# Performance work log

Measured on AMD Instinct MI355X. Metric: run time of the kernel, lower is better.

## Reference

```python
import jax, jax.numpy as jnp
import numpy as np

T0 = 16
EPS = 1.1920929e-07  # torch fp32 finfo eps used by F.rms_norm default

def rmsnorm(v):
    return v * jax.lax.rsqrt(jnp.mean(v * v, axis=-1, keepdims=True) + EPS)

def apply_rotary_emb(x, cos, sin):
    # x: (B, S, H, C); rotate-half style as in source
    d = x.shape[-1] // 2
    x1, x2 = x[..., :d], x[..., d:]
    return jnp.concatenate([x1 * cos + x2 * sin, -x1 * sin + x2 * cos], axis=-1)

def setup_inputs():
    key = jax.random.key(0)
    ks = jax.random.split(key, 8)
    B, T, C, H = 8, 8192, 128, 8
    S = (T0 // 4) * T0 + 1  # 64 selected tokens + 1 sink = 65
    x = jax.random.normal(ks[0], (B, T, C), jnp.float32)
    # RoPE tables over the sink-augmented attention sequence, head_dim/2 = 64
    inv = 1.0 / (10000.0 ** (jnp.arange(C // 2, dtype=jnp.float32) / (C // 2)))
    ang = jnp.arange(S, dtype=jnp.float32)[:, None] * inv[None, :]
    cos = jnp.cos(ang)[None, :, None, :]  # (1, 65, 1, 64)
    sin = jnp.sin(ang)[None, :, None, :]
    sink = 0.02 * jax.random.normal(ks[1], (1, H, C), jnp.float32)
    W_qkvg = 0.02 * jax.random.normal(ks[2], (4 * C * H, C), jnp.float32)
    patch_w = 0.02 * jax.random.normal(ks[3], (T0 * C,), jnp.float32)
    W_out = 0.02 * jax.random.normal(ks[4], (C, H * C), jnp.float32)
    tao = jnp.array([1.2, 1.2], jnp.float32)
    return {"x": x, "cos": cos, "sin": sin, "sink": sink, "W_qkvg": W_qkvg,
            "patch_w": patch_w, "W_out": W_out, "tao": tao}

def reference(x, cos, sin, sink, W_qkvg, patch_w, W_out, tao):
    B, T, C = x.shape
    H = sink.shape[1]
    Np = T // T0  # T chosen as multiple of T0, so pad P = 0
    # --- patch scoring + topk patch selection (patch_toks) ---
    xp = x.reshape(B, Np, T0 * C)
    score = jax.nn.softmax(rmsnorm(xp) @ patch_w, axis=-1)  # (B, Np)
    _, I = jax.lax.top_k(score, T0 // 4)                    # top 4 patches
    I = jnp.sort(I, axis=-1)                                # (B, 4)
    # --- qkvg projection over ALL tokens, then patch-flattened chunk ---
    qkvg = x @ W_qkvg.T                                     # (B, T, 4*C*H)
    qkvg_p = qkvg.reshape(B, Np, 4 * T0 * C * H)
    n = T0 * C * H
    q_p = qkvg_p[..., 0 * n:1 * n]
    k_p = qkvg_p[..., 1 * n:2 * n]
    v_p = qkvg_p[..., 2 * n:3 * n]
    g_p = qkvg_p[..., 3 * n:4 * n]
    def gather(p):  # (B, Np, n) -> (B, 4*T0, H, C) via selected patches
        return jnp.take_along_axis(p, I[:, :, None], axis=1).reshape(B, -1, H, C)
    q, k, v, g = gather(q_p), gather(k_p), gather(v_p), gather(g_p)
    # --- sink token prepend ---
    s = jnp.broadcast_to(sink[:, None], (B, 1, H, C))
    q = jnp.concatenate([s, q], axis=1)  # (B, 65, H, C)
    k = jnp.concatenate([s, k], axis=1)
    v = jnp.concatenate([s, v], axis=1)
    # --- RoPE + RMSNorm + learned temperatures ---
    q = rmsnorm(apply_rotary_emb(q, cos, sin)) * tao[0]
    k = rmsnorm(apply_rotary_emb(k, cos, sin)) * tao[1]
    # --- causal SDPA (scale 1/sqrt(C)), drop sink row ---
    S = q.shape[1]
    att = jnp.einsum('bshc,bthc->bhst', q, k) / jnp.sqrt(jnp.float32(C))
    causal = jnp.tril(jnp.ones((S, S), dtype=bool))
    att = jax.nn.softmax(jnp.where(causal, att, -jnp.inf), axis=-1)
    y = jnp.einsum('bhst,bthc->bshc', att, v)[:, 1:]  # (B, 64, H, C)
    # --- sigmoid gating + output projection ---
    y = y * jax.nn.sigmoid(g)
    return y.reshape(B, y.shape[1], H * C) @ W_out.T  # (B, 64, C)
```

## Files before the change

### kernel.cpp

```cpp
#include <hip/hip_runtime.h>
#include <hip/hip_bf16.h>

#define EPSR 1.1920929e-07f

#define OFF_SCORE 0LL
#define OFF_WQT   8192LL
#define OFF_WO4   532480LL
#define OFF_SEL   663552LL
#define OFF_YG    4757504LL

__device__ __forceinline__ bool is_bf16_in(const void* tao) {
    unsigned int w = *(const unsigned int*)tao;
    return (w >> 16) == (w & 0xffffu);
}

__device__ __forceinline__ float ldin(const void* p, long long i, bool bf) {
    if (bf) return __uint_as_float(((unsigned int)(((const unsigned short*)p)[i])) << 16);
    return ((const float*)p)[i];
}

__device__ __forceinline__ float4 ldin4(const void* p, long long i, bool bf) {
    if (bf) {
        ushort4 u = ((const ushort4*)p)[i >> 2];
        return make_float4(__uint_as_float((unsigned int)u.x << 16),
                           __uint_as_float((unsigned int)u.y << 16),
                           __uint_as_float((unsigned int)u.z << 16),
                           __uint_as_float((unsigned int)u.w << 16));
    }
    return ((const float4*)p)[i >> 2];
}

__global__ __launch_bounds__(256) void k_prep_score(const void* Wq, const void* Wo,
                                                    const void* x, const void* pw,
                                                    const void* tao, float* ws) {
    bool bf = is_bf16_in(tao);
    __shared__ float tile[16448];
    int tid = threadIdx.x;
    if (blockIdx.x < 1024) {
        int lane = tid & 63, wid = tid >> 6;
        int patch = blockIdx.x * 4 + wid;
        long long base = (long long)patch * 2048;
        float ss = 0.f, dt = 0.f;
        #pragma unroll
        for (int i = 0; i < 8; i++) {
            int e = i * 256 + lane * 4;
            float4 v = ldin4(x, base + e, bf);
            float4 w = ldin4(pw, e, bf);
            ss += v.x * v.x + v.y * v.y + v.z * v.z + v.w * v.w;
            dt += v.x * w.x + v.y * w.y + v.z * w.z + v.w * w.w;
        }
        #pragma unroll
        for (int o = 32; o; o >>= 1) { ss += __shfl_xor(ss, o); dt += __shfl_xor(dt, o); }
        if (lane == 0) ws[OFF_SCORE + patch] = dt * rsqrtf(ss * (1.f / 2048.f) + EPSR);
    } else if (blockIdx.x < 1088) {
        float* WqT = ws + OFF_WQT;
        int j0 = (blockIdx.x - 1024) * 64;
        #pragma unroll
        for (int rep = 0; rep < 8; rep++) {
            int jr = rep * 8 + (tid >> 5);
            int c4 = (tid & 31) * 4;
            float4 v = ldin4(Wq, ((long long)(j0 + jr)) * 128 + c4, bf);
            float* t = &tile[jr * 129 + c4];
            t[0] = v.x; t[1] = v.y; t[2] = v.z; t[3] = v.w;
        }
        __syncthreads();
        #pragma unroll
        for (int rep = 0; rep < 8; rep++) {
            int c = rep * 16 + (tid >> 4);
            int jq = (tid & 15) * 4;
            float4 v = make_float4(tile[jq * 129 + c], tile[(jq + 1) * 129 + c],
                                   tile[(jq + 2) * 129 + c], tile[(jq + 3) * 129 + c]);
            *(float4*)&WqT[c * 4096 + j0 + jq] = v;
        }
    } else {
        float* Wo4 = ws + OFF_WO4;
        int co0 = (blockIdx.x - 1088) * 16;
        #pragma unroll
        for (int rep = 0; rep < 16; rep++) {
            float4 v = ldin4(Wo, ((long long)(co0 + rep)) * 1024 + tid * 4, bf);
            *(float4*)&tile[rep * 1028 + tid * 4] = v;
        }
        __syncthreads();
        #pragma unroll
        for (int rep = 0; rep < 16; rep++) {
            int idx = rep * 256 + tid;
            int fg = idx >> 4, co = idx & 15;
            float4 v = *(const float4*)&tile[co * 1028 + fg * 4];
            *(float4*)&Wo4[(fg * 128 + co0 + co) * 4] = v;
        }
    }
}

__global__ __launch_bounds__(256) void k_qkvg(const void* x, const void* tao, float* ws) {
    bool bf = is_bf16_in(tao);
    int blk = blockIdx.x;
    int jc = blk & 15, bp = blk >> 4;
    int b = bp >> 2, p = bp & 3;
    __shared__ float4 xs4[512];
    __shared__ int tok0s;
    int tid = threadIdx.x;
    if (tid < 64) {
        const float4* sp = (const float4*)(ws + OFF_SCORE + b * 512);
        float4 a = sp[tid * 2], c = sp[tid * 2 + 1];
        float v[8];
        v[0] = a.x; v[1] = a.y; v[2] = a.z; v[3] = a.w;
        v[4] = c.x; v[5] = c.y; v[6] = c.z; v[7] = c.w;
        int win[4];
        #pragma unroll
        for (int k = 0; k < 4; k++) {
            float bm = v[0]; int bi = 0;
            #pragma unroll
            for (int i = 1; i < 8; i++) if (v[i] > bm) { bm = v[i]; bi = i; }
            int gi = tid * 8 + bi;
            #pragma unroll
            for (int o = 32; o; o >>= 1) {
                float om = __shfl_xor(bm, o); int oi = __shfl_xor(gi, o);
                if (om > bm || (om == bm && oi < gi)) { bm = om; gi = oi; }
            }
            win[k] = gi;
            if ((gi >> 3) == tid) v[gi & 7] = -INFINITY;
        }
        if (tid == 0) {
            int a0 = win[0], a1 = win[1], a2 = win[2], a3 = win[3], tmp;
            if (a0 > a1) { tmp = a0; a0 = a1; a1 = tmp; }
            if (a2 > a3) { tmp = a2; a2 = a3; a3 = tmp; }
            if (a0 > a2) { tmp = a0; a0 = a2; a2 = tmp; }
            if (a1 > a3) { tmp = a1; a1 = a3; a3 = tmp; }
            if (a1 > a2) { tmp = a1; a1 = a2; a2 = tmp; }
            int sorted[4] = {a0, a1, a2, a3};
            tok0s = sorted[p] * 16;
        }
    }
    __syncthreads();
    int tok0 = tok0s;
    long long xbase = ((long long)(b * 8192 + tok0)) * 128;
    for (int i = tid; i < 512; i += 256)
        xs4[i] = ldin4(x, xbase + i * 4, bf);
    __syncthreads();
    int tg = tid >> 6, jx = tid & 63;
    const float4* WqT4 = (const float4*)(ws + OFF_WQT);
    int wcol = jc * 64 + jx;
    float4 acc[4];
    #pragma unroll
    for (int t = 0; t < 4; t++) acc[t] = make_float4(0.f, 0.f, 0.f, 0.f);
    float4 nw0 = WqT4[0 * 1024 + wcol];
    float4 nw1 = WqT4[1 * 1024 + wcol];
    float4 nw2 = WqT4[2 * 1024 + wcol];
    float4 nw3 = WqT4[3 * 1024 + wcol];
    for (int c4 = 0; c4 < 32; c4++) {
        float4 w0 = nw0, w1 = nw1, w2 = nw2, w3 = nw3;
        if (c4 < 31) {
            nw0 = WqT4[(c4 * 4 + 4) * 1024 + wcol];
            nw1 = WqT4[(c4 * 4 + 5) * 1024 + wcol];
            nw2 = WqT4[(c4 * 4 + 6) * 1024 + wcol];
            nw3 = WqT4[(c4 * 4 + 7) * 1024 + wcol];
        }
        #pragma unroll
        for (int t = 0; t < 4; t++) {
            float4 xv = xs4[(tg * 4 + t) * 32 + c4];
            acc[t].x += xv.x * w0.x + xv.y * w1.x + xv.z * w2.x + xv.w * w3.x;
            acc[t].y += xv.x * w0.y + xv.y * w1.y + xv.z * w2.y + xv.w * w3.y;
            acc[t].z += xv.x * w0.z + xv.y * w1.z + xv.z * w2.z + xv.w * w3.z;
            acc[t].w += xv.x * w0.w + xv.y * w1.w + xv.z * w2.w + xv.w * w3.w;
        }
    }
    float4* sel4 = (float4*)(ws + OFF_SEL);
    #pragma unroll
    for (int t = 0; t < 4; t++)
        sel4[(bp * 16 + tg * 4 + t) * 1024 + wcol] = acc[t];
}

__global__ __launch_bounds__(512, 2) void k_fused(const void* sink, const void* cosp, const void* sinp,
                                                  const void* tao, float* ws) {
    bool bf = is_bf16_in(tao);
    const float* sel = ws + OFF_SEL;
    float* yg = ws + OFF_YG;
    int blk = blockIdx.x;
    int b = blk >> 5, h = (blk >> 2) & 7, qd = blk & 3;
    int bp = b * 4 + qd;
    int smax = qd * 16 + 16;
    int tid = threadIdx.x, lane = tid & 63, wid = tid >> 6;
    __shared__ float qs[16 * 132];
    __shared__ float ks[65 * 132];
    __shared__ float vs[65 * 132];
    __shared__ float att[16 * 68];
    float tao0 = ldin(tao, 0, bf), tao1 = ldin(tao, 1, bf);

    for (int s = wid; s <= smax; s += 8) {
        float cs = ldin(cosp, s * 64 + lane, bf);
        float sn = ldin(sinp, s * 64 + lane, bf);
        #pragma unroll
        for (int which = 0; which < 3; which++) {
            if (which == 0 && !(s > qd * 16)) continue;
            float r1, r2;
            if (s == 0) {
                r1 = ldin(sink, h * 128 + lane, bf);
                r2 = ldin(sink, h * 128 + lane + 64, bf);
            } else {
                int r = s - 1, pp = r >> 4, sl = r & 15;
                int tl = which * 4 + (sl >> 2);
                long long sbase = (((long long)(b * 4 + pp) * 16 + tl) * 4096) + (sl & 3) * 1024 + h * 128;
                r1 = sel[sbase + lane];
                r2 = sel[sbase + lane + 64];
            }
            float o1, o2;
            if (which < 2) {
                o1 = r1 * cs + r2 * sn;
                o2 = -r1 * sn + r2 * cs;
                float ssum = o1 * o1 + o2 * o2;
                #pragma unroll
                for (int o = 32; o; o >>= 1) ssum += __shfl_xor(ssum, o);
                float sc = rsqrtf(ssum * (1.f / 128.f) + EPSR) * (which == 0 ? tao0 : tao1);
                o1 *= sc; o2 *= sc;
            } else {
                o1 = r1; o2 = r2;
            }
            float* dst;
            int row;
            if (which == 0)      { dst = qs; row = s - qd * 16 - 1; }
            else if (which == 1) { dst = ks; row = s; }
            else                 { dst = vs; row = s; }
            dst[row * 132 + lane] = o1;
            dst[row * 132 + lane + 64] = o2;
        }
    }
    __syncthreads();

    {
        int ttiles = qd * 8 + 9;
        int ntiles = 8 * ttiles;
        if (tid < ntiles) {
            int sT = tid & 7, tT = tid >> 3;
            int ls0 = sT * 2;
            int s0g = qd * 16 + 1 + ls0;
            int t0 = tT * 2;
            if (t0 <= s0g + 1) {
                int t1 = (t0 + 1 > smax) ? smax : t0 + 1;
                const float* q0 = &qs[ls0 * 132];
                const float* q1 = &qs[(ls0 + 1) * 132];
                const float* k0 = &ks[t0 * 132];
                const float* k1 = &ks[t1 * 132];
                float a00 = 0.f, a01 = 0.f, a10 = 0.f, a11 = 0.f;
                #pragma unroll 4
                for (int c = 0; c < 128; c += 4) {
                    float4 qa = *(const float4*)(q0 + c);
                    float4 qb = *(const float4*)(q1 + c);
                    float4 ka = *(const float4*)(k0 + c);
                    float4 kb = *(const float4*)(k1 + c);
                    a00 += qa.x * ka.x + qa.y * ka.y + qa.z * ka.z + qa.w * ka.w;
                    a01 += qa.x * kb.x + qa.y * kb.y + qa.z * kb.z + qa.w * kb.w;
                    a10 += qb.x * ka.x + qb.y * ka.y + qb.z * ka.z + qb.w * ka.w;
                    a11 += qb.x * kb.x + qb.y * kb.y + qb.z * kb.z + qb.w * kb.w;
                }
                const float scale = 0.08838834764831845f;
                if (t0 <= s0g)         att[ls0 * 68 + t0] = a00 * scale;
                if (t0 + 1 <= s0g)     att[ls0 * 68 + t0 + 1] = a01 * scale;
                if (t0 <= s0g + 1)     att[(ls0 + 1) * 68 + t0] = a10 * scale;
                if (t0 + 1 <= s0g + 1) att[(ls0 + 1) * 68 + t0 + 1] = a11 * scale;
            }
        }
    }
    __syncthreads();

    for (int ls = wid; ls < 16; ls += 8) {
        int s = qd * 16 + 1 + ls;
        float x1 = (lane <= s) ? __expf(att[ls * 68 + lane]) : 0.f;
        float x2 = (lane == 0 && s == 64) ? __expf(att[ls * 68 + 64]) : 0.f;
        float sum = x1 + x2;
        #pragma unroll
        for (int o = 32; o; o >>= 1) sum += __shfl_xor(sum, o);
        float inv = 1.f / sum;
        att[ls * 68 + lane] = x1 * inv;
        if (lane < 4) att[ls * 68 + 64 + lane] = (lane == 0) ? x2 * inv : 0.f;
    }
    __syncthreads();

    {
        int row = tid >> 5, c0 = (tid & 31) * 4;
        float4 acc = make_float4(0.f, 0.f, 0.f, 0.f);
        const float* ar = &att[row * 68];
        for (int t4 = 0; t4 < smax; t4 += 4) {
            float4 aw = *(const float4*)(ar + t4);
            float4 v0 = *(const float4*)&vs[(t4 + 0) * 132 + c0];
            float4 v1 = *(const float4*)&vs[(t4 + 1) * 132 + c0];
            float4 v2 = *(const float4*)&vs[(t4 + 2) * 132 + c0];
            float4 v3 = *(const float4*)&vs[(t4 + 3) * 132 + c0];
            acc.x += aw.x * v0.x + aw.y * v1.x + aw.z * v2.x + aw.w * v3.x;
            acc.y += aw.x * v0.y + aw.y * v1.y + aw.z * v2.y + aw.w * v3.y;
            acc.z += aw.x * v0.z + aw.y * v1.z + aw.z * v2.z + aw.w * v3.z;
            acc.w += aw.x * v0.w + aw.y * v1.w + aw.z * v2.w + aw.w * v3.w;
        }
        {
            float a = ar[smax];
            float4 vt = *(const float4*)&vs[smax * 132 + c0];
            acc.x += a * vt.x; acc.y += a * vt.y; acc.z += a * vt.z; acc.w += a * vt.w;
        }
        int r = qd * 16 + row;
        int sl = row, tl = 12 + (sl >> 2);
        long long gb = (((long long)bp * 16 + tl) * 4096) + (sl & 3) * 1024 + h * 128 + c0;
        float4 g = *(const float4*)&sel[gb];
        acc.x /= (1.f + __expf(-g.x));
        acc.y /= (1.f + __expf(-g.y));
        acc.z /= (1.f + __expf(-g.z));
        acc.w /= (1.f + __expf(-g.w));
        long long yb = ((long long)(b * 64 + r)) * 1024 + h * 128 + c0;
        *(float4*)&yg[yb] = acc;
    }
}

__global__ __launch_bounds__(256) void k_out(const void* tao, float* ws, void* out) {
    bool bf = is_bf16_in(tao);
    int blk = blockIdx.x;
    int b = blk >> 5, r0 = (blk & 31) * 2;
    __shared__ float4 ygs4[512];
    __shared__ float part[512];
    int tid = threadIdx.x;
    const float4* yg4 = (const float4*)(ws + OFF_YG);
    for (int i = tid; i < 512; i += 256) {
        int row = i >> 8, f4 = i & 255;
        ygs4[i] = yg4[(b * 64 + r0 + row) * 256 + f4];
    }
    __syncthreads();
    int co = tid & 127, fs = tid >> 7;
    const float4* Wo44 = (const float4*)(ws + OFF_WO4);
    float a0 = 0.f, a1 = 0.f;
    int g0 = fs * 128;
    #pragma unroll 2
    for (int g = g0; g < g0 + 128; g++) {
        float4 w = Wo44[g * 128 + co];
        float4 y0 = ygs4[g];
        float4 y1 = ygs4[256 + g];
        a0 += w.x * y0.x + w.y * y0.y + w.z * y0.z + w.w * y0.w;
        a1 += w.x * y1.x + w.y * y1.y + w.z * y1.z + w.w * y1.w;
    }
    part[fs * 256 + co] = a0;
    part[fs * 256 + 128 + co] = a1;
    __syncthreads();
    int row = tid >> 7;
    float v = part[row * 128 + co] + part[256 + row * 128 + co];
    long long o = ((long long)(b * 64 + r0 + row)) * 128 + co;
    if (bf) ((__hip_bfloat16*)out)[o] = __float2bfloat16(v);
    else    ((float*)out)[o] = v;
}

extern "C" void kernel_launch(void* const* d_in, const int* in_sizes, int n_in,
                              void* d_out, int out_size, void* d_ws, size_t ws_size,
                              hipStream_t stream) {
    const void* x    = d_in[0];
    const void* cosp = d_in[1];
    const void* sinp = d_in[2];
    const void* sink = d_in[3];
    const void* Wq   = d_in[4];
    const void* pw   = d_in[5];
    const void* Wo   = d_in[6];
    const void* tao  = d_in[7];
    float* ws = (float*)d_ws;

    k_prep_score<<<dim3(1096), dim3(256), 0, stream>>>(Wq, Wo, x, pw, tao, ws);
    k_qkvg <<<dim3(512), dim3(256), 0, stream>>>(x, tao, ws);
    k_fused<<<dim3(256), dim3(512), 0, stream>>>(sink, cosp, sinp, tao, ws);
    k_out  <<<dim3(256), dim3(256), 0, stream>>>(tao, ws, d_out);
}
```

Before: 147.3 us.

## Split attention into 8-row query chunks, read V from global, retile output projection

The fused attention kernel now splits each (batch, head) into eight 8-query-row blocks instead of four 16-row blocks, which doubles the grid to 512 blocks. It also drops the shared-memory V buffer, reading V rows straight from the workspace during the PV product, and computes the Q and K rotary/normalisation in a single pass so their shuffle reductions are shared. The output projection kernel is re-tiled so each block handles 4 rows and a 64-column half, with each thread producing four outputs over a quarter of the reduction. The aim is to raise parallelism and occupancy and cut shared-memory use. In exchange, K is recomputed more often across blocks and V is read through global/L2 rather than LDS.

```diff
diff --git a/kernel.cpp b/kernel.cpp
--- a/kernel.cpp
+++ b/kernel.cpp
@@ -170,69 +170,71 @@
         sel4[(bp * 16 + tg * 4 + t) * 1024 + wcol] = acc[t];
 }
 
-__global__ __launch_bounds__(512, 2) void k_fused(const void* sink, const void* cosp, const void* sinp,
+__global__ __launch_bounds__(512, 4) void k_fused(const void* sink, const void* cosp, const void* sinp,
                                                   const void* tao, float* ws) {
     bool bf = is_bf16_in(tao);
     const float* sel = ws + OFF_SEL;
     float* yg = ws + OFF_YG;
     int blk = blockIdx.x;
-    int b = blk >> 5, h = (blk >> 2) & 7, qd = blk & 3;
-    int bp = b * 4 + qd;
-    int smax = qd * 16 + 16;
+    int b = blk >> 6, h = (blk >> 3) & 7, o = blk & 7;
+    int smax = o * 8 + 8;
     int tid = threadIdx.x, lane = tid & 63, wid = tid >> 6;
-    __shared__ float qs[16 * 132];
+    __shared__ float qs[8 * 132];
     __shared__ float ks[65 * 132];
-    __shared__ float vs[65 * 132];
-    __shared__ float att[16 * 68];
+    __shared__ float att[8 * 68];
+    __shared__ float sinkv[128];
     float tao0 = ldin(tao, 0, bf), tao1 = ldin(tao, 1, bf);
+
+    if (tid < 128) sinkv[tid] = ldin(sink, h * 128 + tid, bf);
 
     for (int s = wid; s <= smax; s += 8) {
         float cs = ldin(cosp, s * 64 + lane, bf);
         float sn = ldin(sinp, s * 64 + lane, bf);
-        #pragma unroll
-        for (int which = 0; which < 3; which++) {
-            if (which == 0 && !(s > qd * 16)) continue;
-            float r1, r2;
-            if (s == 0) {
-                r1 = ldin(sink, h * 128 + lane, bf);
-                r2 = ldin(sink, h * 128 + lane + 64, bf);
-            } else {
-                int r = s - 1, pp = r >> 4, sl = r & 15;
-                int tl = which * 4 + (sl >> 2);
-                long long sbase = (((long long)(b * 4 + pp) * 16 + tl) * 4096) + (sl & 3) * 1024 + h * 128;
-                r1 = sel[sbase + lane];
-                r2 = sel[sbase + lane + 64];
-            }
-            float o1, o2;
-            if (which < 2) {
-                o1 = r1 * cs + r2 * sn;
-                o2 = -r1 * sn + r2 * cs;
-                float ssum = o1 * o1 + o2 * o2;
-                #pragma unroll
-                for (int o = 32; o; o >>= 1) ssum += __shfl_xor(ssum, o);
-                float sc = rsqrtf(ssum * (1.f / 128.f) + EPSR) * (which == 0 ? tao0 : tao1);
-                o1 *= sc; o2 *= sc;
-            } else {
-                o1 = r1; o2 = r2;
-            }
-            float* dst;
-            int row;
-            if (which == 0)      { dst = qs; row = s - qd * 16 - 1; }
-            else if (which == 1) { dst = ks; row = s; }
-            else                 { dst = vs; row = s; }
-            dst[row * 132 + lane] = o1;
-            dst[row * 132 + lane + 64] = o2;
+        bool doq = (s > o * 8);
+        float kr1, kr2, qr1 = 0.f, qr2 = 0.f;
+        if (s == 0) {
+            kr1 = ldin(sink, h * 128 + lane, bf);
+            kr2 = ldin(sink, h * 128 + lane + 64, bf);
+        } else {
+            int r = s - 1, pp = r >> 4, sl = r & 15;
+            long long kb = (((long long)(b * 4 + pp) * 16 + 4 + (sl >> 2)) * 4096) + (sl & 3) * 1024 + h * 128;
+            kr1 = sel[kb + lane];
+            kr2 = sel[kb + lane + 64];
+            if (doq) {
+                long long qb = (((long long)(b * 4 + pp) * 16 + (sl >> 2)) * 4096) + (sl & 3) * 1024 + h * 128;
+                qr1 = sel[qb + lane];
+                qr2 = sel[qb + lane + 64];
+            }
+        }
+        float k1 = kr1 * cs + kr2 * sn;
+        float k2 = -kr1 * sn + kr2 * cs;
+        float kss = k1 * k1 + k2 * k2;
+        float q1 = qr1 * cs + qr2 * sn;
+        float q2 = -qr1 * sn + qr2 * cs;
+        float qss = q1 * q1 + q2 * q2;
+        #pragma unroll
+        for (int ofs = 32; ofs; ofs >>= 1) {
+            kss += __shfl_xor(kss, ofs);
+            qss += __shfl_xor(qss, ofs);
+        }
+        float ksc = rsqrtf(kss * (1.f / 128.f) + EPSR) * tao1;
+        ks[s * 132 + lane] = k1 * ksc;
+        ks[s * 132 + lane + 64] = k2 * ksc;
+        if (doq) {
+            float qsc = rsqrtf(qss * (1.f / 128.f) + EPSR) * tao0;
+            int lr = s - o * 8 - 1;
+            qs[lr * 132 + lane] = q1 * qsc;
+            qs[lr * 132 + lane + 64] = q2 * qsc;
         }
     }
     __syncthreads();
 
     {
-        int ttiles = qd * 8 + 9;
-        int ntiles = 8 * ttiles;
+        int ntiles = 4 * (4 * o + 5);
         if (tid < ntiles) {
-            int sT = tid & 7, tT = tid >> 3;
+            int sT = tid & 3, tT = tid >> 2;
             int ls0 = sT * 2;
-            int s0g = qd * 16 + 1 + ls0;
+            int s0g = o * 8 + 1 + ls0;
             int t0 = tT * 2;
             if (t0 <= s0g + 1) {
                 int t1 = (t0 + 1 > smax) ? smax : t0 + 1;
@@ -253,57 +255,75 @@
                     a11 += qb.x * kb.x + qb.y * kb.y + qb.z * kb.z + qb.w * kb.w;
                 }
                 const float scale = 0.08838834764831845f;
-                if (t0 <= s0g)         att[ls0 * 68 + t0] = a00 * scale;
-                if (t0 + 1 <= s0g)     att[ls0 * 68 + t0 + 1] = a01 * scale;
-                if (t0 <= s0g + 1)     att[(ls0 + 1) * 68 + t0] = a10 * scale;
+                if (t0 <= s0g)     att[ls0 * 68 + t0] = a00 * scale;
+                if (t0 + 1 <= s0g) att[ls0 * 68 + t0 + 1] = a01 * scale;
+                att[(ls0 + 1) * 68 + t0] = a10 * scale;
                 if (t0 + 1 <= s0g + 1) att[(ls0 + 1) * 68 + t0 + 1] = a11 * scale;
             }
         }
     }
     __syncthreads();
 
-    for (int ls = wid; ls < 16; ls += 8) {
-        int s = qd * 16 + 1 + ls;
+    {
+        int ls = wid;
+        int s = o * 8 + 1 + ls;
         float x1 = (lane <= s) ? __expf(att[ls * 68 + lane]) : 0.f;
         float x2 = (lane == 0 && s == 64) ? __expf(att[ls * 68 + 64]) : 0.f;
         float sum = x1 + x2;
         #pragma unroll
-        for (int o = 32; o; o >>= 1) sum += __shfl_xor(sum, o);
+        for (int ofs = 32; ofs; ofs >>= 1) sum += __shfl_xor(sum, ofs);
         float inv = 1.f / sum;
         att[ls * 68 + lane] = x1 * inv;
         if (lane < 4) att[ls * 68 + 64 + lane] = (lane == 0) ? x2 * inv : 0.f;
     }
     __syncthreads();
 
-    {
+    if (tid < 256) {
         int row = tid >> 5, c0 = (tid & 31) * 4;
+        const float* ar = &att[row * 68];
         float4 acc = make_float4(0.f, 0.f, 0.f, 0.f);
-        const float* ar = &att[row * 68];
-        for (int t4 = 0; t4 < smax; t4 += 4) {
-            float4 aw = *(const float4*)(ar + t4);
-            float4 v0 = *(const float4*)&vs[(t4 + 0) * 132 + c0];
-            float4 v1 = *(const float4*)&vs[(t4 + 1) * 132 + c0];
-            float4 v2 = *(const float4*)&vs[(t4 + 2) * 132 + c0];
-            float4 v3 = *(const float4*)&vs[(t4 + 3) * 132 + c0];
-            acc.x += aw.x * v0.x + aw.y * v1.x + aw.z * v2.x + aw.w * v3.x;
-            acc.y += aw.x * v0.y + aw.y * v1.y + aw.z * v2.y + aw.w * v3.y;
-            acc.z += aw.x * v0.z + aw.y * v1.z + aw.z * v2.z + aw.w * v3.z;
-            acc.w += aw.x * v0.w + aw.y * v1.w + aw.z * v2.w + aw.w * v3.w;
+        {
+            float4 a = *(const float4*)ar;
+            float4 v0 = *(const float4*)&sinkv[c0];
+            acc.x += a.x * v0.x; acc.y += a.x * v0.y; acc.z += a.x * v0.z; acc.w += a.x * v0.w;
+            #pragma unroll
+            for (int j = 1; j < 4; j++) {
+                int r = j - 1;
+                long long vb = (((long long)(b * 4) * 16 + 8 + (r >> 2)) * 4096) + (r & 3) * 1024 + h * 128 + c0;
+                float4 vt = *(const float4*)&sel[vb];
+                float aj = (j == 1) ? a.y : (j == 2) ? a.z : a.w;
+                acc.x += aj * vt.x; acc.y += aj * vt.y; acc.z += aj * vt.z; acc.w += aj * vt.w;
+            }
+        }
+        for (int t4 = 4; t4 <= smax - 4; t4 += 4) {
+            float4 a = *(const float4*)(ar + t4);
+            #pragma unroll
+            for (int j = 0; j < 4; j++) {
+                int r = t4 + j - 1;
+                int pp = r >> 4, sl = r & 15;
+                long long vb = (((long long)(b * 4 + pp) * 16 + 8 + (sl >> 2)) * 4096) + (sl & 3) * 1024 + h * 128 + c0;
+                float4 vt = *(const float4*)&sel[vb];
+                float aj = (j == 0) ? a.x : (j == 1) ? a.y : (j == 2) ? a.z : a.w;
+                acc.x += aj * vt.x; acc.y += aj * vt.y; acc.z += aj * vt.z; acc.w += aj * vt.w;
+            }
         }
         {
             float a = ar[smax];
-            float4 vt = *(const float4*)&vs[smax * 132 + c0];
+            int r = smax - 1;
+            int pp = r >> 4, sl = r & 15;
+            long long vb = (((long long)(b * 4 + pp) * 16 + 8 + (sl >> 2)) * 4096) + (sl & 3) * 1024 + h * 128 + c0;
+            float4 vt = *(const float4*)&sel[vb];
             acc.x += a * vt.x; acc.y += a * vt.y; acc.z += a * vt.z; acc.w += a * vt.w;
         }
-        int r = qd * 16 + row;
-        int sl = row, tl = 12 + (sl >> 2);
-        long long gb = (((long long)bp * 16 + tl) * 4096) + (sl & 3) * 1024 + h * 128 + c0;
+        int rg = o * 8 + row;
+        int pp = rg >> 4, sl = rg & 15, tl = 12 + (sl >> 2);
+        long long gb = (((long long)(b * 4 + pp) * 16 + tl) * 4096) + (sl & 3) * 1024 + h * 128 + c0;
         float4 g = *(const float4*)&sel[gb];
         acc.x /= (1.f + __expf(-g.x));
         acc.y /= (1.f + __expf(-g.y));
         acc.z /= (1.f + __expf(-g.z));
         acc.w /= (1.f + __expf(-g.w));
-        long long yb = ((long long)(b * 64 + r)) * 1024 + h * 128 + c0;
+        long long yb = ((long long)(b * 64 + rg)) * 1024 + h * 128 + c0;
         *(float4*)&yg[yb] = acc;
     }
 }
@@ -311,36 +331,42 @@
 __global__ __launch_bounds__(256) void k_out(const void* tao, float* ws, void* out) {
     bool bf = is_bf16_in(tao);
     int blk = blockIdx.x;
-    int b = blk >> 5, r0 = (blk & 31) * 2;
-    __shared__ float4 ygs4[512];
-    __shared__ float part[512];
+    int b = blk >> 5, rq = (blk >> 1) & 15, ch = blk & 1;
+    int r0 = rq * 4, cbase = ch * 64;
+    __shared__ float4 ylds[4 * 257];
+    __shared__ float part[4][4][64];
     int tid = threadIdx.x;
     const float4* yg4 = (const float4*)(ws + OFF_YG);
-    for (int i = tid; i < 512; i += 256) {
+    for (int i = tid; i < 1024; i += 256) {
         int row = i >> 8, f4 = i & 255;
-        ygs4[i] = yg4[(b * 64 + r0 + row) * 256 + f4];
-    }
-    __syncthreads();
-    int co = tid & 127, fs = tid >> 7;
+        ylds[row * 257 + f4] = yg4[(b * 64 + r0 + row) * 256 + f4];
+    }
+    __syncthreads();
+    int co4 = tid & 15, row = (tid >> 4) & 3, fs = tid >> 6;
     const float4* Wo44 = (const float4*)(ws + OFF_WO4);
-    float a0 = 0.f, a1 = 0.f;
-    int g0 = fs * 128;
+    const float4* yrow = &ylds[row * 257];
+    float a0 = 0.f, a1 = 0.f, a2 = 0.f, a3 = 0.f;
+    int g0 = fs * 64;
     #pragma unroll 2
-    for (int g = g0; g < g0 + 128; g++) {
-        float4 w = Wo44[g * 128 + co];
-        float4 y0 = ygs4[g];
-        float4 y1 = ygs4[256 + g];
-        a0 += w.x * y0.x + w.y * y0.y + w.z * y0.z + w.w * y0.w;
-        a1 += w.x * y1.x + w.y * y1.y + w.z * y1.z + w.w * y1.w;
-    }
-    part[fs * 256 + co] = a0;
-    part[fs * 256 + 128 + co] = a1;
-    __syncthreads();
-    int row = tid >> 7;
-    float v = part[row * 128 + co] + part[256 + row * 128 + co];
-    long long o = ((long long)(b * 64 + r0 + row)) * 128 + co;
-    if (bf) ((__hip_bfloat16*)out)[o] = __float2bfloat16(v);
-    else    ((float*)out)[o] = v;
+    for (int g = g0; g < g0 + 64; g++) {
+        float4 y = yrow[g];
+        const float4* wp = &Wo44[g * 128 + cbase + co4 * 4];
+        float4 w0 = wp[0], w1 = wp[1], w2 = wp[2], w3 = wp[3];
+        a0 += y.x * w0.x + y.y * w0.y + y.z * w0.z + y.w * w0.w;
+        a1 += y.x * w1.x + y.y * w1.y + y.z * w1.z + y.w * w1.w;
+        a2 += y.x * w2.x + y.y * w2.y + y.z * w2.z + y.w * w2.w;
+        a3 += y.x * w3.x + y.y * w3.y + y.z * w3.z + y.w * w3.w;
+    }
+    part[fs][row][co4 * 4 + 0] = a0;
+    part[fs][row][co4 * 4 + 1] = a1;
+    part[fs][row][co4 * 4 + 2] = a2;
+    part[fs][row][co4 * 4 + 3] = a3;
+    __syncthreads();
+    int row2 = tid >> 6, co = tid & 63;
+    float v = part[0][row2][co] + part[1][row2][co] + part[2][row2][co] + part[3][row2][co];
+    long long oidx = ((long long)(b * 64 + r0 + row2)) * 128 + cbase + co;
+    if (bf) ((__hip_bfloat16*)out)[oidx] = __float2bfloat16(v);
+    else    ((float*)out)[oidx] = v;
 }
 
 extern "C" void kernel_launch(void* const* d_in, const int* in_sizes, int n_in,
@@ -358,6 +384,6 @@
 
     k_prep_score<<<dim3(1096), dim3(256), 0, stream>>>(Wq, Wo, x, pw, tao, ws);
     k_qkvg <<<dim3(512), dim3(256), 0, stream>>>(x, tao, ws);
-    k_fused<<<dim3(256), dim3(512), 0, stream>>>(sink, cosp, sinp, tao, ws);
+    k_fused<<<dim3(512), dim3(512), 0, stream>>>(sink, cosp, sinp, tao, ws);
     k_out  <<<dim3(256), dim3(256), 0, stream>>>(tao, ws, d_out);
 }
```

Measured after the change: 146.5 us. Within noise of the previous version (-0.6%).
